# Kernel tuning notes

Measured on AMD Instinct MI355X. Metric: run time of the kernel, lower is better.

Reference implementation:

```python
import jax, jax.numpy as jnp
import numpy as np

B, T, C = 2, 2048, 2048
NH, NKVH = 16, 4
HS = C // NH  # 128
NEG_INF = -1e30


def _rope_freqs(T, hs, base=10000.0):
    inv = 1.0 / (base ** (np.arange(0, hs, 2, dtype=np.float32) / hs))  # [hs/2]
    ang = np.arange(T, dtype=np.float32)[:, None] * inv[None, :]        # [T, hs/2]
    return jnp.asarray(np.cos(ang)), jnp.asarray(np.sin(ang))


def setup_inputs() -> dict:
    key = jax.random.key(0)
    ks = jax.random.split(key, 4)
    x = jax.random.normal(ks[0], (B, T, C), dtype=jnp.float32)
    W_attn = jax.random.normal(ks[1], (C, C + 2 * NKVH * HS), dtype=jnp.float32) * 0.02
    b_attn = jnp.zeros((C + 2 * NKVH * HS,), dtype=jnp.float32)
    W_proj = jax.random.normal(ks[2], (C, C), dtype=jnp.float32) * 0.02
    b_proj = jnp.zeros((C,), dtype=jnp.float32)
    freqs_cos, freqs_sin = _rope_freqs(T, HS)
    return {"x": x, "freqs_cos": freqs_cos, "freqs_sin": freqs_sin,
            "W_attn": W_attn, "b_attn": b_attn, "W_proj": W_proj, "b_proj": b_proj}


def _apply_rope(x, cos, sin):
    # x: [B, T, H, hs]; cos/sin: [T, hs/2] -> broadcast [1, T, 1, hs/2]
    b, t, h, hs = x.shape
    x_ = x.reshape(b, t, h, hs // 2, 2)
    re, im = x_[..., 0], x_[..., 1]
    c = cos[None, :, None, :]
    s = sin[None, :, None, :]
    out_re = re * c - im * s
    out_im = re * s + im * c
    return jnp.stack([out_re, out_im], axis=-1).reshape(b, t, h, hs)


def reference(x, freqs_cos, freqs_sin, W_attn, b_attn, W_proj, b_proj):
    b, t, c = x.shape
    qkv = x @ W_attn + b_attn                                   # [B,T,C+2*nkvh*hs]
    q, k, v = jnp.split(qkv, [c, c + NKVH * HS], axis=2)
    q = q.reshape(b, t, NH, HS)
    k = k.reshape(b, t, NKVH, HS)
    v = v.reshape(b, t, NKVH, HS)
    q = _apply_rope(q, freqs_cos, freqs_sin)
    k = _apply_rope(k, freqs_cos, freqs_sin)
    # group heads: q [B, nkvh, rep, T, hs]; k,v [B, nkvh, T, hs]
    rep = NH // NKVH
    q = q.transpose(0, 2, 1, 3).reshape(b, NKVH, rep, t, HS)
    k = k.transpose(0, 2, 1, 3)
    v = v.transpose(0, 2, 1, 3)
    scale = 1.0 / jnp.sqrt(jnp.asarray(HS, dtype=x.dtype))
    scores = jnp.einsum('bgrth,bgsh->bgrts', q, k) * scale      # [B,g,rep,T,T]
    causal = jnp.tril(jnp.ones((t, t), dtype=bool))
    scores = jnp.where(causal[None, None, None], scores, NEG_INF)
    att = jax.nn.softmax(scores, axis=-1)
    y = jnp.einsum('bgrts,bgsh->bgrth', att, v)                 # [B,g,rep,T,hs]
    y = y.reshape(b, NH, t, HS).transpose(0, 2, 1, 3).reshape(b, t, c)
    return y @ W_proj + b_proj
```

## Files before the change

### kernel.cpp

```cpp
#include <hip/hip_runtime.h>
#include <hip/hip_bf16.h>
#include <stdint.h>

#define B_ 2
#define T_ 2048
#define C_ 2048
#define NH_ 16
#define NKVH_ 4
#define HS_ 128
#define QKV_ 3072
#define NTOK_ 4096

typedef __attribute__((ext_vector_type(4))) float f32x4;
typedef __attribute__((ext_vector_type(16))) float f32x16;
typedef __attribute__((ext_vector_type(8))) short s16x8;

__device__ __forceinline__ short f2bf(float f) {
    union { float f; unsigned u; } v; v.f = f;
    unsigned r = v.u + 0x7FFFu + ((v.u >> 16) & 1u);
    return (short)(r >> 16);
}

__device__ __forceinline__ void async16(const void* g, void* l) {
    __builtin_amdgcn_global_load_lds(
        (const __attribute__((address_space(1))) void*)g,
        (__attribute__((address_space(3))) void*)l, 16, 0, 0);
}

__global__ void cast_bf16_kernel(const float* __restrict__ x, short* __restrict__ out, int n8) {
    int i = blockIdx.x * 256 + threadIdx.x;
    if (i >= n8) return;
    const float4* p = (const float4*)x + (size_t)i * 2;
    float4 a = p[0], b = p[1];
    short o[8] = { f2bf(a.x), f2bf(a.y), f2bf(a.z), f2bf(a.w),
                   f2bf(b.x), f2bf(b.y), f2bf(b.z), f2bf(b.w) };
    *(int4*)(out + (size_t)i * 8) = *(const int4*)o;
}

__global__ void transcast(const float* __restrict__ W, short* __restrict__ WT, int Kd, int Nd) {
    __shared__ float tile[64][65];
    int k0 = blockIdx.x * 64, n0 = blockIdx.y * 64;
    int tid = threadIdx.x;
    int cl = tid & 63, rw = tid >> 6;
    for (int it = 0; it < 16; ++it) {
        int r = it * 4 + rw;
        tile[r][cl] = W[(size_t)(k0 + r) * Nd + n0 + cl];
    }
    __syncthreads();
    for (int it = 0; it < 16; ++it) {
        int n = it * 4 + rw;
        WT[(size_t)(n0 + n) * Kd + k0 + cl] = f2bf(tile[cl][n]);
    }
}

__global__ __launch_bounds__(256, 2) void gemm_bt(
    const short* __restrict__ A, const short* __restrict__ Bt,
    const float* __restrict__ bias, float* __restrict__ Cc,
    int M, int N, int K)
{
    __shared__ short As[128 * 64];
    __shared__ short Bs[128 * 64];
    int tid = threadIdx.x;
    int w = tid >> 6, l = tid & 63;
    int lr = l & 15, lg = l >> 4;
    int bm = blockIdx.x, bn = blockIdx.y;
    int wm = (w >> 1) * 64, wn = (w & 1) * 64;
    f32x4 acc[4][4];
#pragma unroll
    for (int i = 0; i < 4; i++)
#pragma unroll
        for (int j = 0; j < 4; j++) { acc[i][j][0]=0.f; acc[i][j][1]=0.f; acc[i][j][2]=0.f; acc[i][j][3]=0.f; }
    int arow = l >> 3, acol = (l & 7) * 8;
    for (int k0 = 0; k0 < K; k0 += 64) {
#pragma unroll
        for (int i = 0; i < 4; i++) {
            int chunk = w * 4 + i;
            int row = chunk * 8 + arow;
            async16(A  + (size_t)(bm * 128 + row) * K + k0 + acol, (char*)As + chunk * 1024);
            async16(Bt + (size_t)(bn * 128 + row) * K + k0 + acol, (char*)Bs + chunk * 1024);
        }
        __syncthreads();
#pragma unroll
        for (int ks = 0; ks < 2; ks++) {
            s16x8 af[4], bf[4];
#pragma unroll
            for (int mi = 0; mi < 4; mi++)
                af[mi] = *(const s16x8*)&As[(wm + mi * 16 + lr) * 64 + ks * 32 + lg * 8];
#pragma unroll
            for (int ni = 0; ni < 4; ni++)
                bf[ni] = *(const s16x8*)&Bs[(wn + ni * 16 + lr) * 64 + ks * 32 + lg * 8];
#pragma unroll
            for (int mi = 0; mi < 4; mi++)
#pragma unroll
                for (int ni = 0; ni < 4; ni++)
                    acc[mi][ni] = __builtin_amdgcn_mfma_f32_16x16x32_bf16(af[mi], bf[ni], acc[mi][ni], 0, 0, 0);
        }
        __syncthreads();
    }
#pragma unroll
    for (int mi = 0; mi < 4; mi++) {
        int row = bm * 128 + wm + mi * 16 + lg * 4;
#pragma unroll
        for (int ni = 0; ni < 4; ni++) {
            int col = bn * 128 + wn + ni * 16 + lr;
            float bv = bias[col];
#pragma unroll
            for (int j = 0; j < 4; j++)
                Cc[(size_t)(row + j) * N + col] = acc[mi][ni][j] + bv;
        }
    }
}

__global__ void rope_scatter(const float* __restrict__ qkv,
                             const float* __restrict__ fcos, const float* __restrict__ fsin,
                             short* __restrict__ Q, short* __restrict__ Kb)
{
    const float qscale = 0.08838834764831845f;
    int idx = blockIdx.x * 256 + threadIdx.x;
    int tok = idx / 1280, p = idx - tok * 1280;
    if (tok >= NTOK_) return;
    int b = tok >> 11, t = tok & 2047;
    if (p < 1024) {
        int h = p >> 6, i = p & 63;
        const float* src = qkv + (size_t)tok * QKV_ + h * 128 + 2 * i;
        float re = src[0], im = src[1];
        float c = fcos[t * 64 + i], s = fsin[t * 64 + i];
        unsigned lo = (unsigned short)f2bf((re * c - im * s) * qscale);
        unsigned hi = (unsigned short)f2bf((re * s + im * c) * qscale);
        *(unsigned*)(Q + ((size_t)(b * NH_ + h) * T_ + t) * HS_ + 2 * i) = lo | (hi << 16);
    } else {
        int pk = p - 1024; int g = pk >> 6, i = pk & 63;
        const float* src = qkv + (size_t)tok * QKV_ + C_ + g * 128 + 2 * i;
        float re = src[0], im = src[1];
        float c = fcos[t * 64 + i], s = fsin[t * 64 + i];
        unsigned lo = (unsigned short)f2bf(re * c - im * s);
        unsigned hi = (unsigned short)f2bf(re * s + im * c);
        *(unsigned*)(Kb + ((size_t)(b * NKVH_ + g) * T_ + t) * HS_ + 2 * i) = lo | (hi << 16);
    }
}

__global__ void v_transpose(const float* __restrict__ qkv, short* __restrict__ VT) {
    __shared__ float tile[64][65];
    int t0 = blockIdx.x * 64, d0 = blockIdx.y * 64;
    int bg = blockIdx.z; int b = bg >> 2, g = bg & 3;
    int tid = threadIdx.x; int cl = tid & 63, rw = tid >> 6;
    const float* base = qkv + (size_t)(b * T_ + t0) * QKV_ + C_ + NKVH_ * HS_ + g * HS_ + d0;
    for (int it = 0; it < 16; ++it) {
        int r = it * 4 + rw;
        tile[r][cl] = base[(size_t)r * QKV_ + cl];
    }
    __syncthreads();
    short* out = VT + ((size_t)(b * NKVH_ + g) * HS_ + d0) * T_ + t0;
    for (int it = 0; it < 16; ++it) {
        int d = it * 4 + rw;
        out[(size_t)d * T_ + cl] = f2bf(tile[cl][d]);
    }
}

__global__ __launch_bounds__(256, 2) void attn_kernel(
    const short* __restrict__ Qg, const short* __restrict__ Kg,
    const short* __restrict__ VTg, short* __restrict__ Y)
{
    __shared__ short Ks[2][64 * 128];
    __shared__ short VTs[2][128 * 64];
    __shared__ short Ps[4][32 * 64];
    int tid = threadIdx.x, w = tid >> 6, l = tid & 63;
    int l31 = l & 31, hi = l >> 5;
    int yy = blockIdx.y;
    int qt = (yy < 8) ? yy : 23 - yy;
    int bh = blockIdx.x;
    int b = bh >> 4, h = bh & 15, g = h >> 2;
    const short* Qb = Qg + (size_t)(b * NH_ + h) * T_ * HS_;
    const short* Kb = Kg + (size_t)(b * NKVH_ + g) * T_ * HS_;
    const short* Vb = VTg + (size_t)(b * NKVH_ + g) * HS_ * T_;

    auto STAGE = [&](int st, int buf) {
#pragma unroll
        for (int i = 0; i < 4; i++) {
            int chunk = w * 4 + i;
            int poff = chunk * 1024 + l * 16;
            int qoffk = poff ^ (((poff >> 8) & 7) << 4);
            async16(Kb + (size_t)(st * 64 + (qoffk >> 8)) * HS_ + ((qoffk & 255) >> 1),
                    (char*)&Ks[buf][0] + chunk * 1024);
            int qoffv = poff ^ (((poff >> 7) & 7) << 4);
            async16(Vb + (size_t)(qoffv >> 7) * T_ + st * 64 + ((qoffv & 127) >> 1),
                    (char*)&VTs[buf][0] + chunk * 1024);
        }
    };

    int qw = qt * 128 + w * 32;
    int qglob = qw + l31;

    s16x8 qf[8];
#pragma unroll
    for (int dc = 0; dc < 8; dc++)
        qf[dc] = *(const s16x8*)(Qb + (size_t)qglob * HS_ + dc * 16 + hi * 8);

    f32x16 oacc[4];
#pragma unroll
    for (int db = 0; db < 4; db++)
#pragma unroll
        for (int i = 0; i < 16; i++) oacc[db][i] = 0.f;
    float m = -1e30f, lsum = 0.f;
    int nst = 2 * qt + 2;

    STAGE(0, 0);
    __syncthreads();
    int cur = 0;

    for (int st = 0; st < nst; ++st) {
        if (st + 1 < nst) STAGE(st + 1, cur ^ 1);
        if (st * 64 <= qw) {
            const char* KsC = (const char*)&Ks[cur][0];
            const char* VsC = (const char*)&VTs[cur][0];
            char* PsC = (char*)&Ps[w][0];

            f32x16 sacc[2];
            __builtin_amdgcn_s_setprio(1);
#pragma unroll
            for (int sb = 0; sb < 2; sb++) {
                f32x16 a0, a1;
#pragma unroll
                for (int i = 0; i < 16; i++) { a0[i] = 0.f; a1[i] = 0.f; }
#pragma unroll
                for (int dc = 0; dc < 4; dc++) {
                    int lo0 = (sb * 32 + l31) * 256 + dc * 32 + hi * 16;
                    int po0 = lo0 ^ (((lo0 >> 8) & 7) << 4);
                    s16x8 kf0 = *(const s16x8*)(KsC + po0);
                    a0 = __builtin_amdgcn_mfma_f32_32x32x16_bf16(kf0, qf[dc], a0, 0, 0, 0);
                    int lo1 = (sb * 32 + l31) * 256 + (dc + 4) * 32 + hi * 16;
                    int po1 = lo1 ^ (((lo1 >> 8) & 7) << 4);
                    s16x8 kf1 = *(const s16x8*)(KsC + po1);
                    a1 = __builtin_amdgcn_mfma_f32_32x32x16_bf16(kf1, qf[dc + 4], a1, 0, 0, 0);
                }
#pragma unroll
                for (int i = 0; i < 16; i++) a0[i] += a1[i];
                sacc[sb] = a0;
            }
            __builtin_amdgcn_s_setprio(0);
            if (st * 64 + 63 > qw) {
#pragma unroll
                for (int sb = 0; sb < 2; sb++)
#pragma unroll
                    for (int r = 0; r < 16; r++) {
                        int s = st * 64 + sb * 32 + (r & 3) + 8 * (r >> 2) + 4 * hi;
                        if (s > qglob) sacc[sb][r] = -1e30f;
                    }
            }
            float tm = -1e30f;
#pragma unroll
            for (int sb = 0; sb < 2; sb++)
#pragma unroll
                for (int r = 0; r < 16; r++) tm = fmaxf(tm, sacc[sb][r]);
            tm = fmaxf(tm, __shfl_xor(tm, 32));
            if (__any(tm > m)) {
                float mn = fmaxf(m, tm);
                float corr = __expf(m - mn);
                m = mn; lsum *= corr;
#pragma unroll
                for (int db = 0; db < 4; db++)
#pragma unroll
                    for (int r = 0; r < 16; r++) oacc[db][r] *= corr;
            }
#pragma unroll
            for (int sb = 0; sb < 2; sb++)
#pragma unroll
                for (int k = 0; k < 4; k++) {
                    float p0 = __expf(sacc[sb][4 * k]     - m);
                    float p1 = __expf(sacc[sb][4 * k + 1] - m);
                    float p2 = __expf(sacc[sb][4 * k + 2] - m);
                    float p3 = __expf(sacc[sb][4 * k + 3] - m);
                    lsum += (p0 + p1) + (p2 + p3);
                    unsigned w01 = (unsigned short)f2bf(p0) | ((unsigned)(unsigned short)f2bf(p1) << 16);
                    unsigned w23 = (unsigned short)f2bf(p2) | ((unsigned)(unsigned short)f2bf(p3) << 16);
                    uint2 pkv; pkv.x = w01; pkv.y = w23;
                    int sl = sb * 32 + 8 * k + 4 * hi;
                    int lo = l31 * 128 + sl * 2;
                    int po = lo ^ (((lo >> 7) & 7) << 4);
                    *(uint2*)(PsC + po) = pkv;
                }
            __builtin_amdgcn_s_setprio(1);
#pragma unroll
            for (int sc = 0; sc < 4; sc++) {
                unsigned ptmp[4];
                int lp = l31 * 128 + sc * 32 + hi * 16;
                int pp = lp ^ (((lp >> 7) & 7) << 4);
                *(uint2*)&ptmp[0] = *(const uint2*)(PsC + pp);
                *(uint2*)&ptmp[2] = *(const uint2*)(PsC + pp + 8);
                s16x8 pf = *(const s16x8*)ptmp;
#pragma unroll
                for (int db = 0; db < 4; db++) {
                    int lo = (db * 32 + l31) * 128 + sc * 32 + hi * 16;
                    int po = lo ^ (((lo >> 7) & 7) << 4);
                    s16x8 vf = *(const s16x8*)(VsC + po);
                    oacc[db] = __builtin_amdgcn_mfma_f32_32x32x16_bf16(vf, pf, oacc[db], 0, 0, 0);
                }
            }
            __builtin_amdgcn_s_setprio(0);
        }
        __syncthreads();
        cur ^= 1;
    }

    lsum += __shfl_xor(lsum, 32);
    float inv = 1.0f / lsum;
    short* Yrow = Y + (size_t)(b * T_ + qglob) * C_ + h * 128;
#pragma unroll
    for (int db = 0; db < 4; db++)
#pragma unroll
        for (int pr = 0; pr < 8; pr++) {
            unsigned u0 = (unsigned short)f2bf(oacc[db][2 * pr] * inv);
            unsigned u1 = (unsigned short)f2bf(oacc[db][2 * pr + 1] * inv);
            int d = db * 32 + ((2 * pr) & 3) + 8 * (pr >> 1) + 4 * hi;
            *(unsigned*)(Yrow + d) = u0 | (u1 << 16);
        }
}

extern "C" void kernel_launch(void* const* d_in, const int* in_sizes, int n_in,
                              void* d_out, int out_size, void* d_ws, size_t ws_size,
                              hipStream_t stream)
{
    const float* x      = (const float*)d_in[0];
    const float* fcos   = (const float*)d_in[1];
    const float* fsin   = (const float*)d_in[2];
    const float* W_attn = (const float*)d_in[3];
    const float* b_attn = (const float*)d_in[4];
    const float* W_proj = (const float*)d_in[5];
    const float* b_proj = (const float*)d_in[6];
    float* out = (float*)d_out;
    char* ws = (char*)d_ws;

    short* xb  = (short*)(ws + 0);
    float* qkv = (float*)(ws + 16777216);
    short* y   = (short*)(ws + 16777216);
    short* WpT = (short*)(ws + 33554432);
    short* WaT = (short*)(ws + 67108864);
    short* Qb  = (short*)(ws + 67108864);
    short* Kb  = (short*)(ws + 83886080);
    short* VT  = (short*)(ws + 88080384);

    cast_bf16_kernel<<<4096, 256, 0, stream>>>(x, xb, NTOK_ * C_ / 8);
    transcast<<<dim3(32, 48), 256, 0, stream>>>(W_attn, WaT, C_, QKV_);
    gemm_bt<<<dim3(32, 24), 256, 0, stream>>>(xb, WaT, b_attn, qkv, NTOK_, QKV_, C_);
    rope_scatter<<<20480, 256, 0, stream>>>(qkv, fcos, fsin, Qb, Kb);
    v_transpose<<<dim3(32, 2, 8), 256, 0, stream>>>(qkv, VT);
    transcast<<<dim3(32, 32), 256, 0, stream>>>(W_proj, WpT, C_, C_);
    attn_kernel<<<dim3(32, 16), 256, 0, stream>>>(Qb, Kb, VT, y);
    gemm_bt<<<dim3(32, 16), 256, 0, stream>>>(y, WpT, b_proj, out, NTOK_, C_, C_);
}
```

Before: 223.9 us.

## Fuse RoPE, Q/K scatter and V transpose into QKV GEMM epilogue

Replaces the generic QKV GEMM, which wrote an fp32 qkv buffer, with a specialized GEMM whose epilogue applies bias, RoPE (pairing lanes via shuffle) and the query scale. It then writes bf16 Q/K in head-major layout and V transposed directly. This removes two kernel launches and the write plus re-read of a 48MB fp32 intermediate. The cost is scattered 2-byte stores for Q/K and per-element cos/sin loads in the epilogue, and the workspace layout is reorganized.

```diff
diff --git a/kernel.cpp b/kernel.cpp
--- a/kernel.cpp
+++ b/kernel.cpp
@@ -111,49 +111,96 @@
     }
 }
 
-__global__ void rope_scatter(const float* __restrict__ qkv,
-                             const float* __restrict__ fcos, const float* __restrict__ fsin,
-                             short* __restrict__ Q, short* __restrict__ Kb)
+__global__ __launch_bounds__(256, 2) void gemm_qkv(
+    const short* __restrict__ A, const short* __restrict__ Bt,
+    const float* __restrict__ bias,
+    const float* __restrict__ fcos, const float* __restrict__ fsin,
+    short* __restrict__ Q, short* __restrict__ Kb, short* __restrict__ VT)
 {
-    const float qscale = 0.08838834764831845f;
-    int idx = blockIdx.x * 256 + threadIdx.x;
-    int tok = idx / 1280, p = idx - tok * 1280;
-    if (tok >= NTOK_) return;
-    int b = tok >> 11, t = tok & 2047;
-    if (p < 1024) {
-        int h = p >> 6, i = p & 63;
-        const float* src = qkv + (size_t)tok * QKV_ + h * 128 + 2 * i;
-        float re = src[0], im = src[1];
-        float c = fcos[t * 64 + i], s = fsin[t * 64 + i];
-        unsigned lo = (unsigned short)f2bf((re * c - im * s) * qscale);
-        unsigned hi = (unsigned short)f2bf((re * s + im * c) * qscale);
-        *(unsigned*)(Q + ((size_t)(b * NH_ + h) * T_ + t) * HS_ + 2 * i) = lo | (hi << 16);
+    __shared__ short As[128 * 64];
+    __shared__ short Bs[128 * 64];
+    const int K = C_;
+    int tid = threadIdx.x;
+    int w = tid >> 6, l = tid & 63;
+    int lr = l & 15, lg = l >> 4;
+    int bm = blockIdx.x, bn = blockIdx.y;
+    int wm = (w >> 1) * 64, wn = (w & 1) * 64;
+    f32x4 acc[4][4];
+#pragma unroll
+    for (int i = 0; i < 4; i++)
+#pragma unroll
+        for (int j = 0; j < 4; j++) { acc[i][j][0]=0.f; acc[i][j][1]=0.f; acc[i][j][2]=0.f; acc[i][j][3]=0.f; }
+    int arow = l >> 3, acol = (l & 7) * 8;
+    for (int k0 = 0; k0 < K; k0 += 64) {
+#pragma unroll
+        for (int i = 0; i < 4; i++) {
+            int chunk = w * 4 + i;
+            int row = chunk * 8 + arow;
+            async16(A  + (size_t)(bm * 128 + row) * K + k0 + acol, (char*)As + chunk * 1024);
+            async16(Bt + (size_t)(bn * 128 + row) * K + k0 + acol, (char*)Bs + chunk * 1024);
+        }
+        __syncthreads();
+#pragma unroll
+        for (int ks = 0; ks < 2; ks++) {
+            s16x8 af[4], bf[4];
+#pragma unroll
+            for (int mi = 0; mi < 4; mi++)
+                af[mi] = *(const s16x8*)&As[(wm + mi * 16 + lr) * 64 + ks * 32 + lg * 8];
+#pragma unroll
+            for (int ni = 0; ni < 4; ni++)
+                bf[ni] = *(const s16x8*)&Bs[(wn + ni * 16 + lr) * 64 + ks * 32 + lg * 8];
+#pragma unroll
+            for (int mi = 0; mi < 4; mi++)
+#pragma unroll
+                for (int ni = 0; ni < 4; ni++)
+                    acc[mi][ni] = __builtin_amdgcn_mfma_f32_16x16x32_bf16(af[mi], bf[ni], acc[mi][ni], 0, 0, 0);
+        }
+        __syncthreads();
+    }
+    int b = bm >> 4;
+    int tt0 = (bm & 15) * 128 + wm;
+    const float qsc = 0.08838834764831845f;
+    if (bn < 20) {
+        bool isQ = (bn < 16);
+        short* Ob = isQ ? (Q + (size_t)(b * NH_ + bn) * T_ * HS_)
+                        : (Kb + (size_t)(b * NKVH_ + (bn - 16)) * T_ * HS_);
+        float sc = isQ ? qsc : 1.0f;
+#pragma unroll
+        for (int ni = 0; ni < 4; ni++) {
+            int d = wn + ni * 16 + lr;
+            int i = d >> 1;
+            float ssign = (d & 1) ? 1.0f : -1.0f;
+            float bv = bias[bn * 128 + d];
+#pragma unroll
+            for (int mi = 0; mi < 4; mi++) {
+                int ttb = tt0 + mi * 16 + lg * 4;
+#pragma unroll
+                for (int j = 0; j < 4; j++) {
+                    float v = acc[mi][ni][j] + bv;
+                    float prt = __shfl_xor(v, 1);
+                    int tt = ttb + j;
+                    float c = fcos[tt * 64 + i], s = fsin[tt * 64 + i];
+                    float outv = (v * c + ssign * prt * s) * sc;
+                    Ob[(size_t)tt * HS_ + d] = f2bf(outv);
+                }
+            }
+        }
     } else {
-        int pk = p - 1024; int g = pk >> 6, i = pk & 63;
-        const float* src = qkv + (size_t)tok * QKV_ + C_ + g * 128 + 2 * i;
-        float re = src[0], im = src[1];
-        float c = fcos[t * 64 + i], s = fsin[t * 64 + i];
-        unsigned lo = (unsigned short)f2bf(re * c - im * s);
-        unsigned hi = (unsigned short)f2bf(re * s + im * c);
-        *(unsigned*)(Kb + ((size_t)(b * NKVH_ + g) * T_ + t) * HS_ + 2 * i) = lo | (hi << 16);
-    }
-}
-
-__global__ void v_transpose(const float* __restrict__ qkv, short* __restrict__ VT) {
-    __shared__ float tile[64][65];
-    int t0 = blockIdx.x * 64, d0 = blockIdx.y * 64;
-    int bg = blockIdx.z; int b = bg >> 2, g = bg & 3;
-    int tid = threadIdx.x; int cl = tid & 63, rw = tid >> 6;
-    const float* base = qkv + (size_t)(b * T_ + t0) * QKV_ + C_ + NKVH_ * HS_ + g * HS_ + d0;
-    for (int it = 0; it < 16; ++it) {
-        int r = it * 4 + rw;
-        tile[r][cl] = base[(size_t)r * QKV_ + cl];
-    }
-    __syncthreads();
-    short* out = VT + ((size_t)(b * NKVH_ + g) * HS_ + d0) * T_ + t0;
-    for (int it = 0; it < 16; ++it) {
-        int d = it * 4 + rw;
-        out[(size_t)d * T_ + cl] = f2bf(tile[cl][d]);
+        int g = bn - 20;
+        short* Vb = VT + (size_t)(b * NKVH_ + g) * HS_ * T_;
+#pragma unroll
+        for (int ni = 0; ni < 4; ni++) {
+            int d = wn + ni * 16 + lr;
+            float bv = bias[bn * 128 + d];
+#pragma unroll
+            for (int mi = 0; mi < 4; mi++) {
+                int ttb = tt0 + mi * 16 + lg * 4;
+                short pk4[4];
+#pragma unroll
+                for (int j = 0; j < 4; j++) pk4[j] = f2bf(acc[mi][ni][j] + bv);
+                *(int2*)(Vb + (size_t)d * T_ + ttb) = *(const int2*)pk4;
+            }
+        }
     }
 }
 
@@ -331,19 +378,16 @@
     char* ws = (char*)d_ws;
 
     short* xb  = (short*)(ws + 0);
-    float* qkv = (float*)(ws + 16777216);
     short* y   = (short*)(ws + 16777216);
     short* WpT = (short*)(ws + 33554432);
+    short* Qb  = (short*)(ws + 41943040);
+    short* Kb  = (short*)(ws + 58720256);
+    short* VT  = (short*)(ws + 62914560);
     short* WaT = (short*)(ws + 67108864);
-    short* Qb  = (short*)(ws + 67108864);
-    short* Kb  = (short*)(ws + 83886080);
-    short* VT  = (short*)(ws + 88080384);
 
     cast_bf16_kernel<<<4096, 256, 0, stream>>>(x, xb, NTOK_ * C_ / 8);
     transcast<<<dim3(32, 48), 256, 0, stream>>>(W_attn, WaT, C_, QKV_);
-    gemm_bt<<<dim3(32, 24), 256, 0, stream>>>(xb, WaT, b_attn, qkv, NTOK_, QKV_, C_);
-    rope_scatter<<<20480, 256, 0, stream>>>(qkv, fcos, fsin, Qb, Kb);
-    v_transpose<<<dim3(32, 2, 8), 256, 0, stream>>>(qkv, VT);
+    gemm_qkv<<<dim3(32, 24), 256, 0, stream>>>(xb, WaT, b_attn, fcos, fsin, Qb, Kb, VT);
     transcast<<<dim3(32, 32), 256, 0, stream>>>(W_proj, WpT, C_, C_);
     attn_kernel<<<dim3(32, 16), 256, 0, stream>>>(Qb, Kb, VT, y);
     gemm_bt<<<dim3(32, 16), 256, 0, stream>>>(y, WpT, b_proj, out, NTOK_, C_, C_);
```

Measured after the change: 208.3 us. 7.0% less time.
